# Kernel optimization log

Hardware: AMD Instinct MI355X
Metric: run time of the kernel (lower is better)

Reference implementation:

```python
import jax, jax.numpy as jnp
import numpy as np

N_HEADS = 16
ROPE_BASE = 10000.0

def rotate_half(x):
    x1, x2 = jnp.split(x, 2, axis=-1)
    return jnp.concatenate([-x2, x1], axis=-1)

def rope_tables(T, D, dtype):
    inv_freq = 1.0 / (ROPE_BASE ** (np.arange(0, D, 2, dtype=np.float32) / D))
    t = np.arange(T, dtype=np.float32)
    freqs = np.outer(t, inv_freq)            # [T, D/2]
    emb = np.concatenate([freqs, freqs], -1)  # [T, D]
    return jnp.asarray(np.cos(emb), dtype), jnp.asarray(np.sin(emb), dtype)

def setup_inputs() -> dict:
    key = jax.random.key(0)
    ks = jax.random.split(key, 5)
    B, T, C, D = 2, 2048, 1024, 64
    s = 0.02
    return {
        "x":  jax.random.normal(ks[0], (B, T, C), jnp.float32),
        "Wq": jax.random.normal(ks[1], (C, C), jnp.float32) * s,
        "Wk": jax.random.normal(ks[2], (C, D), jnp.float32) * s,
        "Wv": jax.random.normal(ks[3], (C, D), jnp.float32) * s,
        "Wo": jax.random.normal(ks[4], (C, C), jnp.float32) * s,
    }

def reference(x, Wq, Wk, Wv, Wo):
    B, T, C = x.shape
    H = N_HEADS
    D = C // H
    scale = D ** -0.5
    q = (x @ Wq).reshape(B, T, H, D).transpose(0, 2, 1, 3)  # [B,H,T,D]
    k = x @ Wk                                              # [B,T,D] single KV head
    v = x @ Wv                                              # [B,T,D]
    cos, sin = rope_tables(T, D, x.dtype)                   # [T,D]
    q = q * cos + rotate_half(q) * sin                      # broadcast over B,H
    k = k * cos + rotate_half(k) * sin                      # broadcast over B
    # MQA causal attention: shared K/V head broadcast to all query heads
    scores = jnp.einsum('bhqd,bkd->bhqk', q, k) * scale     # [B,H,T,T]
    causal = jnp.tril(jnp.ones((T, T), bool))
    scores = jnp.where(causal, scores, jnp.finfo(scores.dtype).min)
    attn = jax.nn.softmax(scores, axis=-1)
    out = jnp.einsum('bhqk,bkd->bhqd', attn, v)             # [B,H,T,D]
    out = out.transpose(0, 2, 1, 3).reshape(B, T, C)
    return out @ Wo
```

## Files before the change

### kernel.cpp

```cpp
#include <hip/hip_runtime.h>
#include <hip/hip_bf16.h>

typedef _Float16 f16;
typedef __attribute__((ext_vector_type(8))) _Float16 f16x8;
typedef __attribute__((ext_vector_type(4))) _Float16 f16x4;
typedef __attribute__((ext_vector_type(4))) float f32x4;

#define MFMA16(a, b, c) __builtin_amdgcn_mfma_f32_16x16x32_f16(a, b, c, 0, 0, 0)

__device__ __forceinline__ void gload_lds16(const void* g, void* l)
{
    __builtin_amdgcn_global_load_lds(
        (const __attribute__((address_space(1))) unsigned int*)g,
        (__attribute__((address_space(3))) unsigned int*)l, 16, 0, 0);
}

__global__ __launch_bounds__(256) void cvt_all_kernel(const float* __restrict__ x, const float* __restrict__ Wq,
                                                      const float* __restrict__ Wk, const float* __restrict__ Wv,
                                                      const float* __restrict__ Wo, f16* __restrict__ xb,
                                                      f16* __restrict__ WallT, f16* __restrict__ WoT)
{
    int i = blockIdx.x * 256 + threadIdx.x;
    if (i < 1048576) {
        float4 v = ((const float4*)x)[i];
        f16x4 o;
        o[0] = (f16)v.x; o[1] = (f16)v.y; o[2] = (f16)v.z; o[3] = (f16)v.w;
        *(f16x4*)(xb + 4 * (size_t)i) = o;
        return;
    }
    const float* src;
    f16* dstbase;
    int n4, k4, ldN;
    if (i < 1114112) {
        int j = i - 1048576;
        n4 = (j & 255) * 4; k4 = (j >> 8) * 4;
        src = Wq; ldN = 1024; dstbase = WallT + (size_t)n4 * 1024;
    } else if (i < 1122304) {
        int j = i - 1114112;
        int p4 = (j & 31) * 4; k4 = (j >> 5) * 4;
        if (p4 < 64) {
            n4 = (p4 >= 16 && p4 < 48) ? (p4 ^ 48) : p4;
            src = Wk;
        } else {
            n4 = p4 - 64;
            src = Wv;
        }
        ldN = 64; dstbase = WallT + (size_t)(1024 + p4) * 1024;
    } else {
        int j = i - 1122304;
        n4 = (j & 255) * 4; k4 = (j >> 8) * 4;
        src = Wo; ldN = 1024; dstbase = WoT + (size_t)n4 * 1024;
    }
    float4 v0 = *(const float4*)(src + (size_t)(k4 + 0) * ldN + n4);
    float4 v1 = *(const float4*)(src + (size_t)(k4 + 1) * ldN + n4);
    float4 v2 = *(const float4*)(src + (size_t)(k4 + 2) * ldN + n4);
    float4 v3 = *(const float4*)(src + (size_t)(k4 + 3) * ldN + n4);
    float a0[4] = {v0.x, v0.y, v0.z, v0.w};
    float a1[4] = {v1.x, v1.y, v1.z, v1.w};
    float a2[4] = {v2.x, v2.y, v2.z, v2.w};
    float a3[4] = {v3.x, v3.y, v3.z, v3.w};
#pragma unroll
    for (int jj = 0; jj < 4; ++jj) {
        f16x4 o;
        o[0] = (f16)a0[jj]; o[1] = (f16)a1[jj]; o[2] = (f16)a2[jj]; o[3] = (f16)a3[jj];
        *(f16x4*)(dstbase + (size_t)jj * 1024 + k4) = o;
    }
}

template<int MODE>
__global__ __launch_bounds__(256) void gemm_bt(const f16* __restrict__ A, const f16* __restrict__ Bt,
                                               void* __restrict__ Cv, f16* __restrict__ kout, f16* __restrict__ vout,
                                               int NBX)
{
    __shared__ __align__(16) f16 As[128 * 64];
    __shared__ __align__(16) f16 Bs[64 * 64];
    int id = blockIdx.x;
    int qn = gridDim.x >> 3;
    int lin = (id & 7) * qn + (id >> 3);
    int bx = lin % NBX, by = lin / NBX;
    int tid = threadIdx.x, lane = tid & 63, wid = tid >> 6;
    int wr = wid >> 1, wc = wid & 1;
    int lrow = lane & 15, gq = lane >> 4;
    f32x4 acc[4][2];
#pragma unroll
    for (int fm = 0; fm < 4; ++fm)
#pragma unroll
        for (int fn = 0; fn < 2; ++fn) acc[fm][fn] = (f32x4){0.f, 0.f, 0.f, 0.f};

    for (int kt = 0; kt < 16; ++kt) {
        int k0 = kt * 64;
#pragma unroll
        for (int i = 0; i < 4; ++i) {
            int c = wid * 4 + i;
            int row = c * 8 + (lane >> 3);
            int slot = (lane & 7) ^ (row & 7);
            gload_lds16(A + (size_t)(by * 128 + row) * 1024 + k0 + slot * 8, &As[c * 512 + lane * 8]);
        }
#pragma unroll
        for (int i = 0; i < 2; ++i) {
            int c = wid * 2 + i;
            int row = c * 8 + (lane >> 3);
            int slot = (lane & 7) ^ (row & 7);
            gload_lds16(Bt + (size_t)(bx * 64 + row) * 1024 + k0 + slot * 8, &Bs[c * 512 + lane * 8]);
        }
        __syncthreads();
#pragma unroll
        for (int ks = 0; ks < 2; ++ks) {
            f16x8 af[4], bf[2];
#pragma unroll
            for (int fm = 0; fm < 4; ++fm) {
                int row = wr * 64 + fm * 16 + lrow;
                int slot = (ks * 4 + gq) ^ (row & 7);
                af[fm] = *(const f16x8*)&As[row * 64 + slot * 8];
            }
#pragma unroll
            for (int fn = 0; fn < 2; ++fn) {
                int row = wc * 32 + fn * 16 + lrow;
                int slot = (ks * 4 + gq) ^ (row & 7);
                bf[fn] = *(const f16x8*)&Bs[row * 64 + slot * 8];
            }
#pragma unroll
            for (int fm = 0; fm < 4; ++fm)
#pragma unroll
                for (int fn = 0; fn < 2; ++fn)
                    acc[fm][fn] = MFMA16(af[fm], bf[fn], acc[fm][fn]);
        }
        __syncthreads();
    }
    if constexpr (MODE == 1) {
        float* C = (float*)Cv;
#pragma unroll
        for (int fm = 0; fm < 4; ++fm)
#pragma unroll
            for (int fn = 0; fn < 2; ++fn)
#pragma unroll
                for (int r = 0; r < 4; ++r) {
                    int row = by * 128 + wr * 64 + fm * 16 + gq * 4 + r;
                    int col = bx * 64 + wc * 32 + fn * 16 + lrow;
                    C[(size_t)row * 1024 + col] = acc[fm][fn][r];
                }
    } else {
        if (bx < 16) {
            f16* C = (f16*)Cv;
#pragma unroll
            for (int fm = 0; fm < 4; ++fm)
#pragma unroll
                for (int fn = 0; fn < 2; ++fn)
#pragma unroll
                    for (int r = 0; r < 4; ++r) {
                        int row = by * 128 + wr * 64 + fm * 16 + gq * 4 + r;
                        int col = bx * 64 + wc * 32 + fn * 16 + lrow;
                        C[(size_t)row * 1024 + col] = (f16)acc[fm][fn][r];
                    }
        } else if (bx == 16) {
            const float L2B = 13.287712379549449f / 64.0f;
            int i = wc * 16 + lrow;
            float invf = exp2f(-(float)(2 * i) * L2B);
#pragma unroll
            for (int fm = 0; fm < 4; ++fm)
#pragma unroll
                for (int r = 0; r < 4; ++r) {
                    int row = by * 128 + wr * 64 + fm * 16 + gq * 4 + r;
                    float t = (float)(row & 2047);
                    float ss, cc;
                    sincosf(t * invf, &ss, &cc);
                    float x1 = acc[fm][0][r], x2 = acc[fm][1][r];
                    kout[(size_t)row * 64 + i]      = (f16)(x1 * cc - x2 * ss);
                    kout[(size_t)row * 64 + i + 32] = (f16)(x2 * cc + x1 * ss);
                }
        } else {
#pragma unroll
            for (int fm = 0; fm < 4; ++fm)
#pragma unroll
                for (int fn = 0; fn < 2; ++fn) {
                    int d = wc * 32 + fn * 16 + lrow;
                    int rowbase = by * 128 + wr * 64 + fm * 16 + gq * 4;
                    f16x4 pw;
#pragma unroll
                    for (int r = 0; r < 4; ++r) pw[r] = (f16)acc[fm][fn][r];
                    *(f16x4*)&vout[(size_t)d * 4096 + rowbase] = pw;
                }
        }
    }
}

#define SOFTMAX(S, MM, LL, OO, PSF) do {                                            \
    float mx = fmaxf(fmaxf(fmaxf(S[0][0],S[0][1]),fmaxf(S[0][2],S[0][3])),          \
                     fmaxf(fmaxf(S[1][0],S[1][1]),fmaxf(S[1][2],S[1][3])));         \
    mx = fmaxf(mx, fmaxf(fmaxf(fmaxf(S[2][0],S[2][1]),fmaxf(S[2][2],S[2][3])),      \
                         fmaxf(fmaxf(S[3][0],S[3][1]),fmaxf(S[3][2],S[3][3]))));    \
    mx = fmaxf(mx, __shfl_xor(mx, 16));                                             \
    mx = fmaxf(mx, __shfl_xor(mx, 32));                                             \
    if (!__all(mx <= MM + 3.0f)) {                                                  \
        float mn = fmaxf(MM, mx);                                                   \
        float alpha = exp2f(MM - mn);                                               \
        MM = mn; LL *= alpha;                                                       \
        float av0 = __shfl(alpha, g * 4 + 0), av1 = __shfl(alpha, g * 4 + 1);       \
        float av2 = __shfl(alpha, g * 4 + 2), av3 = __shfl(alpha, g * 4 + 3);       \
        _Pragma("unroll")                                                           \
        for (int dt = 0; dt < 4; ++dt) {                                            \
            OO[dt][0] *= av0; OO[dt][1] *= av1; OO[dt][2] *= av2; OO[dt][3] *= av3; \
        }                                                                           \
    }                                                                               \
    float rs = 0.f;                                                                 \
    _Pragma("unroll")                                                               \
    for (int tt = 0; tt < 4; ++tt) {                                                \
        f16x4 pw;                                                                   \
        _Pragma("unroll")                                                           \
        for (int r = 0; r < 4; ++r) {                                               \
            float pp = exp2f(S[tt][r] - MM); S[tt][r] = pp; pw[r] = (f16)pp;        \
        }                                                                           \
        rs += (S[tt][0] + S[tt][1]) + (S[tt][2] + S[tt][3]);                        \
        *(f16x4*)&PSF[lrow * 64 + ((tt * 16 + g * 4) ^ swl)] = pw;                  \
    }                                                                               \
    LL += rs;                                                                       \
} while (0)

__global__ __launch_bounds__(256, 4) void attn_kernel(const f16* __restrict__ q, const f16* __restrict__ k,
                                                      const f16* __restrict__ vt, f16* __restrict__ ao,
                                                      char* __restrict__ partial)
{
    constexpr int T = 2048;
    int c = blockIdx.x, bh = blockIdx.y;
    int b = bh >> 4, h = bh & 15;
    int qt, ch;
    if (c < 16)      { qt = 16 + c; ch = 0; }
    else if (c < 32) { qt = c;      ch = 1; }
    else             { qt = 47 - c; ch = 0; }
    int nt = qt + 1;
    int nch = (qt >= 16) ? 2 : 1;
    int tbeg = ch * 16;
    int tend = min(nt, tbeg + 16);

    int tid = threadIdx.x, lane = tid & 63, wid = tid >> 6;
    int lrow = lane & 15, g = lane >> 4;
    int qw = qt * 64 + wid * 16;
    int swl = (lrow & 7) << 3;

    __shared__ __align__(16) f16 Ks[2][64 * 64];
    __shared__ __align__(16) f16 Vs[2][64 * 64];
    __shared__ __align__(16) f16 PsB[4][16 * 64];

    const f16* qrow = q + (size_t)(b * T + qw + lrow) * 1024 + h * 64;
    f16x8 x0 = *(const f16x8*)&qrow[g * 8];
    f16x8 x1 = *(const f16x8*)&qrow[g * 8 + 32];
    f16x8 qf0, qf1;
    {
        const float qsc = 0.125f * 1.4426950408889634f;
        const float L2B = 13.287712379549449f / 64.0f;
        float t_ = (float)(qw + lrow);
#pragma unroll
        for (int j = 0; j < 8; ++j) {
            int i = g * 8 + j;
            float invf = exp2f(-(float)(2 * i) * L2B);
            float ss, cc;
            sincosf(t_ * invf, &ss, &cc);
            float a0 = (float)x0[j], a1 = (float)x1[j];
            qf0[j] = (f16)((a0 * cc - a1 * ss) * qsc);
            qf1[j] = (f16)((a1 * cc + a0 * ss) * qsc);
        }
    }

    float m = -1e30f, l = 0.f;
    f32x4 o[4];
#pragma unroll
    for (int dt = 0; dt < 4; ++dt) o[dt] = (f32x4){0.f, 0.f, 0.f, 0.f};

    const f16* kbase = k + (size_t)b * T * 64;
    const f16* vtbase = vt + (size_t)b * T;

    int srow_lo = lane >> 3, sslot = lane & 7;
#define STAGE(buf, t) do {                                                                   \
    _Pragma("unroll")                                                                        \
    for (int i_ = 0; i_ < 2; ++i_) {                                                         \
        int c2 = wid * 2 + i_;                                                               \
        int row = c2 * 8 + srow_lo;                                                          \
        int slot = sslot ^ (row & 7);                                                        \
        gload_lds16(kbase + (size_t)((t) * 64 + row) * 64 + slot * 8,                        \
                    &Ks[buf][c2 * 512 + lane * 8]);                                          \
        gload_lds16(vtbase + (size_t)row * 4096 + (t) * 64 + slot * 8,                       \
                    &Vs[buf][c2 * 512 + lane * 8]);                                          \
    }                                                                                        \
} while (0)

    STAGE(0, tbeg);
    __syncthreads();
    int cur = 0;

    for (int t = tbeg; t < tend; ++t) {
        if (t + 1 < tend) STAGE(cur ^ 1, t + 1);
        f16* Ps = &PsB[wid][0];
        const f16* Kc = &Ks[cur][0];
        const f16* Vc = &Vs[cur][0];

        f32x4 s[4];
#pragma unroll
        for (int tt = 0; tt < 4; ++tt) {
            f16x8 kf0 = *(const f16x8*)&Kc[(tt * 16 + lrow) * 64 + ((g * 8) ^ swl)];
            f16x8 kf1 = *(const f16x8*)&Kc[(tt * 16 + lrow) * 64 + ((32 + g * 8) ^ swl)];
            f32x4 z = (f32x4){0.f, 0.f, 0.f, 0.f};
            z = MFMA16(kf0, qf0, z);
            z = MFMA16(kf1, qf1, z);
            s[tt] = z;
        }
        if (t == nt - 1) {
            int qab = qw + lrow;
            int kb0 = t * 64 + g * 4;
#pragma unroll
            for (int tt = 0; tt < 4; ++tt)
#pragma unroll
                for (int r = 0; r < 4; ++r)
                    if (kb0 + tt * 16 + r > qab) s[tt][r] = -1e30f;
        }
        SOFTMAX(s, m, l, o, Ps);
#pragma unroll
        for (int chk = 0; chk < 2; ++chk) {
            f16x8 pf = *(const f16x8*)&Ps[lrow * 64 + ((chk * 32 + g * 8) ^ swl)];
#pragma unroll
            for (int dt = 0; dt < 4; ++dt) {
                f16x8 vf = *(const f16x8*)&Vc[(dt * 16 + lrow) * 64 + ((chk * 32 + g * 8) ^ swl)];
                o[dt] = MFMA16(pf, vf, o[dt]);
            }
        }
        __syncthreads();
        cur ^= 1;
    }
#undef STAGE
    l += __shfl_xor(l, 16);
    l += __shfl_xor(l, 32);
    float lv[4];
#pragma unroll
    for (int rr = 0; rr < 4; ++rr) lv[rr] = __shfl(l, g * 4 + rr);

    if (nch == 1) {
#pragma unroll
        for (int rr = 0; rr < 4; ++rr) {
            float inv = 1.f / lv[rr];
            int qab = qw + g * 4 + rr;
#pragma unroll
            for (int dt = 0; dt < 4; ++dt)
                ao[(size_t)(b * T + qab) * 1024 + h * 64 + dt * 16 + lrow] = (f16)(o[dt][rr] * inv);
        }
    } else {
        char* slot = partial + ((size_t)(bh * 16 + (qt - 16)) * 2 + ch) * 8704;
        f16* op = (f16*)slot;
        float* mp = (float*)(slot + 8192);
        float* lp = mp + 64;
#pragma unroll
        for (int rr = 0; rr < 4; ++rr) {
            int row = wid * 16 + g * 4 + rr;
#pragma unroll
            for (int dt = 0; dt < 4; ++dt)
                op[row * 64 + dt * 16 + lrow] = (f16)o[dt][rr];
        }
        if (g == 0) { mp[wid * 16 + lrow] = m; lp[wid * 16 + lrow] = l; }
    }
}

__global__ __launch_bounds__(256) void combine_kernel(const char* __restrict__ partial, f16* __restrict__ ao)
{
    constexpr int T = 2048;
    int qt = 16 + blockIdx.x, bh = blockIdx.y;
    int b = bh >> 4, h = bh & 15;
    int tid = threadIdx.x;
    int row = tid >> 2, dp = (tid & 3) * 16;
    const char* s0 = partial + ((size_t)(bh * 16 + (qt - 16)) * 2) * 8704;
    const char* s1 = s0 + 8704;
    const f16* o0 = (const f16*)s0; const float* m0 = (const float*)(s0 + 8192); const float* l0 = m0 + 64;
    const f16* o1 = (const f16*)s1; const float* m1 = (const float*)(s1 + 8192); const float* l1 = m1 + 64;
    float mm0 = m0[row], mm1 = m1[row];
    float M = fmaxf(mm0, mm1);
    float a0 = exp2f(mm0 - M), a1 = exp2f(mm1 - M);
    float inv = 1.f / (l0[row] * a0 + l1[row] * a1);
    f16x8 u0 = ((const f16x8*)(o0 + row * 64 + dp))[0];
    f16x8 u1 = ((const f16x8*)(o0 + row * 64 + dp))[1];
    f16x8 w0 = ((const f16x8*)(o1 + row * 64 + dp))[0];
    f16x8 w1 = ((const f16x8*)(o1 + row * 64 + dp))[1];
    f16x8 r0, r1;
#pragma unroll
    for (int j = 0; j < 8; ++j) {
        r0[j] = (f16)(((float)u0[j] * a0 + (float)w0[j] * a1) * inv);
        r1[j] = (f16)(((float)u1[j] * a0 + (float)w1[j] * a1) * inv);
    }
    f16* dst = ao + (size_t)(b * T + qt * 64 + row) * 1024 + h * 64 + dp;
    *(f16x8*)dst = r0;
    *(f16x8*)(dst + 8) = r1;
}

extern "C" void kernel_launch(void* const* d_in, const int* in_sizes, int n_in,
                              void* d_out, int out_size, void* d_ws, size_t ws_size,
                              hipStream_t stream)
{
    (void)in_sizes; (void)n_in; (void)out_size; (void)ws_size;
    const float* x  = (const float*)d_in[0];
    const float* Wq = (const float*)d_in[1];
    const float* Wk = (const float*)d_in[2];
    const float* Wv = (const float*)d_in[3];
    const float* Wo = (const float*)d_in[4];
    float* out = (float*)d_out;

    char* w = (char*)d_ws;
    size_t off = 0;
    auto alloc = [&](size_t bytes) -> void* {
        void* p = (void*)(w + off);
        off += (bytes + 255) & ~(size_t)255;
        return p;
    };
    f16* xb    = (f16*)alloc(4194304ull * 2);
    f16* WallT = (f16*)alloc(1179648ull * 2);
    f16* WoT   = (f16*)alloc(1048576ull * 2);
    f16* qg    = (f16*)alloc(4194304ull * 2);
    f16* krp   = (f16*)alloc(262144ull * 2);
    f16* vt    = (f16*)alloc(262144ull * 2);
    f16* ao    = (f16*)alloc(4194304ull * 2);
    char* partial = (char*)xb;

    cvt_all_kernel<<<4640, 256, 0, stream>>>(x, Wq, Wk, Wv, Wo, xb, WallT, WoT);
    gemm_bt<0><<<576, 256, 0, stream>>>(xb, WallT, qg, krp, vt, 18);
    attn_kernel<<<dim3(48, 32), 256, 0, stream>>>(qg, krp, vt, ao, partial);
    combine_kernel<<<dim3(16, 32), 256, 0, stream>>>(partial, ao);
    gemm_bt<1><<<512, 256, 0, stream>>>(ao, WoT, out, nullptr, nullptr, 16);
}
```

Baseline: 110.0 us.

## Process two query heads per attention block to reuse staged K/V tiles

Each attention workgroup now handles two heads (h and h+8) sharing the single MQA K/V head, so every K/V tile staged into LDS feeds twice as many MFMAs and the grid halves. This cuts global K/V traffic and staging overhead per unit of work, at the cost of doubled accumulator registers (occupancy hint lowered from 4 to 3) and fewer workgroups to fill the GPU. It also adds s_setprio around the MFMA sections to favour matrix-issue waves.

```diff
diff --git a/kernel.cpp b/kernel.cpp
--- a/kernel.cpp
+++ b/kernel.cpp
@@ -216,13 +216,13 @@
     LL += rs;                                                                       \
 } while (0)
 
-__global__ __launch_bounds__(256, 4) void attn_kernel(const f16* __restrict__ q, const f16* __restrict__ k,
+__global__ __launch_bounds__(256, 3) void attn_kernel(const f16* __restrict__ q, const f16* __restrict__ k,
                                                       const f16* __restrict__ vt, f16* __restrict__ ao,
                                                       char* __restrict__ partial)
 {
     constexpr int T = 2048;
-    int c = blockIdx.x, bh = blockIdx.y;
-    int b = bh >> 4, h = bh & 15;
+    int c = blockIdx.x, y = blockIdx.y;
+    int b = y >> 3, hA = y & 7, hB = hA + 8;
     int qt, ch;
     if (c < 16)      { qt = 16 + c; ch = 0; }
     else if (c < 32) { qt = c;      ch = 1; }
@@ -239,12 +239,15 @@
 
     __shared__ __align__(16) f16 Ks[2][64 * 64];
     __shared__ __align__(16) f16 Vs[2][64 * 64];
-    __shared__ __align__(16) f16 PsB[4][16 * 64];
-
-    const f16* qrow = q + (size_t)(b * T + qw + lrow) * 1024 + h * 64;
-    f16x8 x0 = *(const f16x8*)&qrow[g * 8];
-    f16x8 x1 = *(const f16x8*)&qrow[g * 8 + 32];
-    f16x8 qf0, qf1;
+    __shared__ __align__(16) f16 PsM[4][2][16 * 64];
+
+    const f16* qrowA = q + (size_t)(b * T + qw + lrow) * 1024 + hA * 64;
+    const f16* qrowB = qrowA + (hB - hA) * 64;
+    f16x8 xA0 = *(const f16x8*)&qrowA[g * 8];
+    f16x8 xA1 = *(const f16x8*)&qrowA[g * 8 + 32];
+    f16x8 xB0 = *(const f16x8*)&qrowB[g * 8];
+    f16x8 xB1 = *(const f16x8*)&qrowB[g * 8 + 32];
+    f16x8 qfA0, qfA1, qfB0, qfB1;
     {
         const float qsc = 0.125f * 1.4426950408889634f;
         const float L2B = 13.287712379549449f / 64.0f;
@@ -255,16 +258,19 @@
             float invf = exp2f(-(float)(2 * i) * L2B);
             float ss, cc;
             sincosf(t_ * invf, &ss, &cc);
-            float a0 = (float)x0[j], a1 = (float)x1[j];
-            qf0[j] = (f16)((a0 * cc - a1 * ss) * qsc);
-            qf1[j] = (f16)((a1 * cc + a0 * ss) * qsc);
-        }
-    }
-
-    float m = -1e30f, l = 0.f;
-    f32x4 o[4];
-#pragma unroll
-    for (int dt = 0; dt < 4; ++dt) o[dt] = (f32x4){0.f, 0.f, 0.f, 0.f};
+            float a0 = (float)xA0[j], a1 = (float)xA1[j];
+            qfA0[j] = (f16)((a0 * cc - a1 * ss) * qsc);
+            qfA1[j] = (f16)((a1 * cc + a0 * ss) * qsc);
+            float b0 = (float)xB0[j], b1 = (float)xB1[j];
+            qfB0[j] = (f16)((b0 * cc - b1 * ss) * qsc);
+            qfB1[j] = (f16)((b1 * cc + b0 * ss) * qsc);
+        }
+    }
+
+    float mA = -1e30f, lA = 0.f, mB = -1e30f, lB = 0.f;
+    f32x4 oA[4], oB[4];
+#pragma unroll
+    for (int dt = 0; dt < 4; ++dt) { oA[dt] = (f32x4){0.f,0.f,0.f,0.f}; oB[dt] = (f32x4){0.f,0.f,0.f,0.f}; }
 
     const f16* kbase = k + (size_t)b * T * 64;
     const f16* vtbase = vt + (size_t)b * T;
@@ -289,20 +295,27 @@
 
     for (int t = tbeg; t < tend; ++t) {
         if (t + 1 < tend) STAGE(cur ^ 1, t + 1);
-        f16* Ps = &PsB[wid][0];
+        f16* PsA = &PsM[wid][0][0];
+        f16* PsBf = &PsM[wid][1][0];
         const f16* Kc = &Ks[cur][0];
         const f16* Vc = &Vs[cur][0];
 
-        f32x4 s[4];
+        f32x4 sA[4], sB[4];
+        __builtin_amdgcn_s_setprio(1);
 #pragma unroll
         for (int tt = 0; tt < 4; ++tt) {
             f16x8 kf0 = *(const f16x8*)&Kc[(tt * 16 + lrow) * 64 + ((g * 8) ^ swl)];
             f16x8 kf1 = *(const f16x8*)&Kc[(tt * 16 + lrow) * 64 + ((32 + g * 8) ^ swl)];
             f32x4 z = (f32x4){0.f, 0.f, 0.f, 0.f};
-            z = MFMA16(kf0, qf0, z);
-            z = MFMA16(kf1, qf1, z);
-            s[tt] = z;
-        }
+            z = MFMA16(kf0, qfA0, z);
+            z = MFMA16(kf1, qfA1, z);
+            sA[tt] = z;
+            z = (f32x4){0.f, 0.f, 0.f, 0.f};
+            z = MFMA16(kf0, qfB0, z);
+            z = MFMA16(kf1, qfB1, z);
+            sB[tt] = z;
+        }
+        __builtin_amdgcn_s_setprio(0);
         if (t == nt - 1) {
             int qab = qw + lrow;
             int kb0 = t * 64 + g * 4;
@@ -310,50 +323,62 @@
             for (int tt = 0; tt < 4; ++tt)
 #pragma unroll
                 for (int r = 0; r < 4; ++r)
-                    if (kb0 + tt * 16 + r > qab) s[tt][r] = -1e30f;
-        }
-        SOFTMAX(s, m, l, o, Ps);
+                    if (kb0 + tt * 16 + r > qab) { sA[tt][r] = -1e30f; sB[tt][r] = -1e30f; }
+        }
+        SOFTMAX(sA, mA, lA, oA, PsA);
+        SOFTMAX(sB, mB, lB, oB, PsBf);
+        __builtin_amdgcn_s_setprio(1);
 #pragma unroll
         for (int chk = 0; chk < 2; ++chk) {
-            f16x8 pf = *(const f16x8*)&Ps[lrow * 64 + ((chk * 32 + g * 8) ^ swl)];
+            f16x8 pfA = *(const f16x8*)&PsA[lrow * 64 + ((chk * 32 + g * 8) ^ swl)];
+            f16x8 pfB = *(const f16x8*)&PsBf[lrow * 64 + ((chk * 32 + g * 8) ^ swl)];
 #pragma unroll
             for (int dt = 0; dt < 4; ++dt) {
                 f16x8 vf = *(const f16x8*)&Vc[(dt * 16 + lrow) * 64 + ((chk * 32 + g * 8) ^ swl)];
-                o[dt] = MFMA16(pf, vf, o[dt]);
+                oA[dt] = MFMA16(pfA, vf, oA[dt]);
+                oB[dt] = MFMA16(pfB, vf, oB[dt]);
             }
         }
+        __builtin_amdgcn_s_setprio(0);
         __syncthreads();
         cur ^= 1;
     }
 #undef STAGE
-    l += __shfl_xor(l, 16);
-    l += __shfl_xor(l, 32);
-    float lv[4];
-#pragma unroll
-    for (int rr = 0; rr < 4; ++rr) lv[rr] = __shfl(l, g * 4 + rr);
+    lA += __shfl_xor(lA, 16); lA += __shfl_xor(lA, 32);
+    lB += __shfl_xor(lB, 16); lB += __shfl_xor(lB, 32);
 
     if (nch == 1) {
 #pragma unroll
         for (int rr = 0; rr < 4; ++rr) {
-            float inv = 1.f / lv[rr];
+            float invA = 1.f / __shfl(lA, g * 4 + rr);
+            float invB = 1.f / __shfl(lB, g * 4 + rr);
             int qab = qw + g * 4 + rr;
-#pragma unroll
-            for (int dt = 0; dt < 4; ++dt)
-                ao[(size_t)(b * T + qab) * 1024 + h * 64 + dt * 16 + lrow] = (f16)(o[dt][rr] * inv);
+            size_t rowoff = (size_t)(b * T + qab) * 1024;
+#pragma unroll
+            for (int dt = 0; dt < 4; ++dt) {
+                ao[rowoff + hA * 64 + dt * 16 + lrow] = (f16)(oA[dt][rr] * invA);
+                ao[rowoff + hB * 64 + dt * 16 + lrow] = (f16)(oB[dt][rr] * invB);
+            }
         }
     } else {
-        char* slot = partial + ((size_t)(bh * 16 + (qt - 16)) * 2 + ch) * 8704;
-        f16* op = (f16*)slot;
-        float* mp = (float*)(slot + 8192);
-        float* lp = mp + 64;
+        int bhA = b * 16 + hA, bhB = b * 16 + hB;
+        char* slotA = partial + ((size_t)(bhA * 16 + (qt - 16)) * 2 + ch) * 8704;
+        char* slotB = partial + ((size_t)(bhB * 16 + (qt - 16)) * 2 + ch) * 8704;
+        f16* opA = (f16*)slotA; float* mpA = (float*)(slotA + 8192); float* lpA = mpA + 64;
+        f16* opB = (f16*)slotB; float* mpB = (float*)(slotB + 8192); float* lpB = mpB + 64;
 #pragma unroll
         for (int rr = 0; rr < 4; ++rr) {
             int row = wid * 16 + g * 4 + rr;
 #pragma unroll
-            for (int dt = 0; dt < 4; ++dt)
-                op[row * 64 + dt * 16 + lrow] = (f16)o[dt][rr];
-        }
-        if (g == 0) { mp[wid * 16 + lrow] = m; lp[wid * 16 + lrow] = l; }
+            for (int dt = 0; dt < 4; ++dt) {
+                opA[row * 64 + dt * 16 + lrow] = (f16)oA[dt][rr];
+                opB[row * 64 + dt * 16 + lrow] = (f16)oB[dt][rr];
+            }
+        }
+        if (g == 0) {
+            mpA[wid * 16 + lrow] = mA; lpA[wid * 16 + lrow] = lA;
+            mpB[wid * 16 + lrow] = mB; lpB[wid * 16 + lrow] = lB;
+        }
     }
 }
 
@@ -417,7 +442,7 @@
 
     cvt_all_kernel<<<4640, 256, 0, stream>>>(x, Wq, Wk, Wv, Wo, xb, WallT, WoT);
     gemm_bt<0><<<576, 256, 0, stream>>>(xb, WallT, qg, krp, vt, 18);
-    attn_kernel<<<dim3(48, 32), 256, 0, stream>>>(qg, krp, vt, ao, partial);
+    attn_kernel<<<dim3(48, 16), 256, 0, stream>>>(qg, krp, vt, ao, partial);
     combine_kernel<<<dim3(16, 32), 256, 0, stream>>>(partial, ao);
     gemm_bt<1><<<512, 256, 0, stream>>>(ao, WoT, out, nullptr, nullptr, 16);
 }
```

Result: faster. 100.2 us (-9.0%).
